# Kernel tuning notes

Hardware: AMD Instinct MI355X
Metric: run time of the kernel (lower is better)

The kernel has to match this reference:

```python
import jax, jax.numpy as jnp
import numpy as np

GAMMA = 0.99
NUM_QUANTILES = 50
STEP_TYPE_LAST = 2
HUBER_DELTA = 1.0

T, B, Q = 128, 512, NUM_QUANTILES


def setup_inputs() -> dict:
    key = jax.random.key(0)
    k1, k2, k3, k4, k5 = jax.random.split(key, 5)
    return {
        "reward": jax.random.normal(k1, (T, B), dtype=jnp.float32),
        "step_type": jax.random.randint(k2, (T, B), 0, 3, dtype=jnp.int32),
        "discount": jax.random.uniform(k3, (T, B), dtype=jnp.float32),
        "value": jax.random.normal(k4, (T, B, Q), dtype=jnp.float32),
        "target_value": jax.random.normal(k5, (T, B, Q), dtype=jnp.float32),
    }


def discounted_return(rewards, values, step_types, discounts):
    """alf value_ops.discounted_return: backward-in-time recurrence.

    rewards/step_types/discounts: [T, B]; values: [T, B, Q].
    Returns [T-1, B, Q]. rets[T-1]=values[T-1];
    rets[t] = is_last[t]*values[t] + (1-is_last[t])*(discounts[t+1]*rets[t+1] + rewards[t+1]).
    """
    is_last = (step_types == STEP_TYPE_LAST).astype(values.dtype)[..., None]  # [T,B,1]
    r = rewards[..., None]    # [T,B,1]
    d = discounts[..., None]  # [T,B,1]

    def step(carry, xs):
        is_last_t, v_t, r_tp1, d_tp1 = xs
        acc = carry * d_tp1 + r_tp1
        ret = is_last_t * v_t + (1.0 - is_last_t) * acc
        return ret, ret

    init = values[-1]
    xs = (is_last[:-1], values[:-1], r[1:], d[1:])
    _, rets = jax.lax.scan(step, init, xs, reverse=True)
    return rets  # [T-1, B, Q]


def huber(x):
    ax = jnp.abs(x)
    return jnp.where(ax <= HUBER_DELTA, 0.5 * x * x, HUBER_DELTA * (ax - 0.5 * HUBER_DELTA))


def reference(reward, step_type, discount, value, target_value):
    # td_lambda == 1.0 -> full discounted return (computed with no grad / detached)
    returns = jax.lax.stop_gradient(
        discounted_return(reward, target_value, step_type, discount * GAMMA))  # [T-1,B,Q]
    v = value[:-1]  # [T-1,B,Q]

    q = returns.shape[-1]
    tau = (jnp.arange(q, dtype=value.dtype) + 0.5) / q  # [Q] cdf midpoints

    # diff[..., i, j] = target_quantile_i - estimated_quantile_j
    diff = returns[..., :, None] - v[..., None, :]  # [T-1,B,Qt,Qe]
    weight = jnp.abs(tau - (jax.lax.stop_gradient(diff) < 0).astype(diff.dtype))
    loss = weight * huber(diff)
    # sum_over_quantiles=True: mean over target quantiles, sum over estimate quantiles
    loss = loss.mean(axis=-2).sum(axis=-1)  # [T-1,B]
    # tensor_extend_zero: append a zero row for the last time step -> [T,B]
    loss = jnp.concatenate([loss, jnp.zeros_like(loss[-1:])], axis=0)
    return loss
```

## Files before the change

### kernel.cpp

```cpp
#include <hip/hip_runtime.h>

#define GAMMA 0.99f
constexpr int T_DIM = 128;
constexpr int B_DIM = 512;
constexpr int Q_DIM = 50;
constexpr int NROW  = (T_DIM - 1) * B_DIM;
constexpr int SLOT  = 52;
constexpr int R_BLK = 20;
constexpr int KEEP  = -1;
constexpr int GRID_LOSS = (NROW + R_BLK - 1) / R_BLK;

__global__ void __launch_bounds__(128) coeff_kernel(
    const float* __restrict__ reward,
    const int*   __restrict__ step_type,
    const float* __restrict__ discount,
    float* __restrict__ alpha,
    float* __restrict__ beta,
    int*   __restrict__ anchor,
    float* __restrict__ out) {
  __shared__ float sp[128], sqa[128], sqb[128];
  __shared__ int   snv[128];
  const int t = threadIdx.x;
  const int b = blockIdx.x;

  float p, qa, qb; int nv;
  if (t < T_DIM - 1) {
    const bool  last = (step_type[t * B_DIM + b] == 2);
    const float d    = GAMMA * discount[(t + 1) * B_DIM + b];
    const float r    = reward[(t + 1) * B_DIM + b];
    p  = last ? 0.0f : d;
    qa = last ? 1.0f : 0.0f;
    qb = last ? 0.0f : r;
    nv = last ? t    : KEEP;
  } else {
    p = 1.0f; qa = 0.0f; qb = 0.0f; nv = KEEP;
    out[(T_DIM - 1) * B_DIM + b] = 0.0f;
  }
  sp[t] = p; sqa[t] = qa; sqb[t] = qb; snv[t] = nv;
  __syncthreads();

#pragma unroll
  for (int off = 1; off < 128; off <<= 1) {
    const bool act = (t + off) < 128;
    float p2 = 1.0f, qa2 = 0.0f, qb2 = 0.0f; int nv2 = KEEP;
    if (act) { p2 = sp[t+off]; qa2 = sqa[t+off]; qb2 = sqb[t+off]; nv2 = snv[t+off]; }
    __syncthreads();
    if (act) {
      qa = fmaf(p, qa2, qa);
      qb = fmaf(p, qb2, qb);
      p  = p * p2;
      nv = (nv == KEEP) ? nv2 : nv;
      sp[t] = p; sqa[t] = qa; sqb[t] = qb; snv[t] = nv;
    }
    __syncthreads();
  }

  if (t < T_DIM - 1) {
    const int row = (b << 7) + t;
    alpha[row]  = p + qa;
    beta[row]   = qb;
    anchor[row] = (nv == KEEP) ? (T_DIM - 1) : nv;
  }
}

__global__ void __launch_bounds__(256) loss_kernel(
    const float* __restrict__ value,
    const float* __restrict__ tv,
    const float* __restrict__ alpha,
    const float* __restrict__ beta,
    const int*   __restrict__ anchor,
    float*       __restrict__ out) {
  __shared__ __align__(16) float sret[R_BLK * SLOT];
  __shared__ float pacc[R_BLK * SLOT];

  const int tid = threadIdx.x;
  const int r0  = blockIdx.x * R_BLK;

  for (int e = tid; e < R_BLK * Q_DIM; e += 256) {
    const int lr  = e / Q_DIM;
    const int i   = e - lr * Q_DIM;
    const int row = r0 + lr;
    float rv = 0.0f;
    if (row < NROW) {
      const int b  = row & (B_DIM - 1);
      const int t  = row >> 9;
      const int ci = (b << 7) + t;
      const int n  = anchor[ci];
      rv = fmaf(alpha[ci], tv[(n * B_DIM + b) * Q_DIM + i], beta[ci]);
    }
    sret[lr * SLOT + i] = rv;
  }
  __syncthreads();

  const bool act   = tid < 5 * Q_DIM;
  const int  r_off = tid / Q_DIM;
  const int  j     = tid - r_off * Q_DIM;
  const float tm05 = ((float)j + 0.5f) * (1.0f / Q_DIM) - 0.5f;

  if (act) {
    float vv[4];
#pragma unroll
    for (int rb = 0; rb < 4; ++rb)
      vv[rb] = value[(r0 + rb * 5) * Q_DIM + tid];

#pragma unroll
    for (int rb = 0; rb < 4; ++rb) {
      const int lr = rb * 5 + r_off;
      const float* rp = &sret[lr * SLOT];
      const float v = vv[rb];

      float s1 = 0.0f, s2 = 0.0f;
      auto pair = [&](float reti) {
        const float d = reti - v;
        const float c = __builtin_amdgcn_fmed3f(d, -1.0f, 1.0f);
        const float e = fmaf(-0.5f, c, d);
        s1 = fmaf(e, c, s1);
        s2 = fmaf(e, fabsf(c), s2);
      };
#pragma unroll
      for (int i0 = 0; i0 < 48; i0 += 4) {
        const float4 rr = *reinterpret_cast<const float4*>(rp + i0);
        pair(rr.x); pair(rr.y); pair(rr.z); pair(rr.w);
      }
      {
        const float2 rr = *reinterpret_cast<const float2*>(rp + 48);
        pair(rr.x); pair(rr.y);
      }
      pacc[lr * SLOT + j] = fmaf(tm05, s2, 0.5f * s1);
    }
  }
  __syncthreads();

  const int w    = tid >> 6;
  const int lane = tid & 63;
#pragma unroll
  for (int k = 0; k < 5; ++k) {
    const int lr   = w * 5 + k;
    const int grow = r0 + lr;
    float x = (lane < Q_DIM) ? pacc[lr * SLOT + lane] : 0.0f;
#pragma unroll
    for (int off = 32; off > 0; off >>= 1)
      x += __shfl_xor(x, off, 64);
    if (lane == 0 && grow < NROW)
      out[grow] = x * (1.0f / Q_DIM);
  }
}

extern "C" void kernel_launch(void* const* d_in, const int* in_sizes, int n_in,
                              void* d_out, int out_size, void* d_ws, size_t ws_size,
                              hipStream_t stream) {
  const float* reward       = (const float*)d_in[0];
  const int*   step_type    = (const int*)  d_in[1];
  const float* discount     = (const float*)d_in[2];
  const float* value        = (const float*)d_in[3];
  const float* target_value = (const float*)d_in[4];
  float* out = (float*)d_out;

  float* alpha  = (float*)d_ws;
  float* beta   = alpha + B_DIM * 128;
  int*   anchor = (int*)(beta + B_DIM * 128);

  coeff_kernel<<<B_DIM, 128, 0, stream>>>(reward, step_type, discount,
                                          alpha, beta, anchor, out);

  loss_kernel<<<GRID_LOSS, 256, 0, stream>>>(value, target_value,
                                             alpha, beta, anchor, out);
}
```

Before: 101.5 us.

## Fuse coefficient scan and quantile loss into one per-batch kernel

Merges the coefficient prefix-scan kernel and the loss kernel into a single kernel with one 1024-thread block per batch column. Alpha, beta and anchor now stay in shared memory, so the workspace round trip and the second launch go away. Each block computes all 127 time steps for its batch index. In exchange the grid shrinks to 512 large blocks using about 53KB of LDS, which limits occupancy. The value and target_value accesses also become strided across time within a block.

```diff
diff --git a/kernel.cpp b/kernel.cpp
--- a/kernel.cpp
+++ b/kernel.cpp
@@ -4,145 +4,115 @@
 constexpr int T_DIM = 128;
 constexpr int B_DIM = 512;
 constexpr int Q_DIM = 50;
-constexpr int NROW  = (T_DIM - 1) * B_DIM;
+constexpr int TRET  = 127;
 constexpr int SLOT  = 52;
-constexpr int R_BLK = 20;
+constexpr int NSLOT = TRET * Q_DIM;
 constexpr int KEEP  = -1;
-constexpr int GRID_LOSS = (NROW + R_BLK - 1) / R_BLK;
 
-__global__ void __launch_bounds__(128) coeff_kernel(
+__global__ void __launch_bounds__(1024) fused_kernel(
     const float* __restrict__ reward,
     const int*   __restrict__ step_type,
     const float* __restrict__ discount,
-    float* __restrict__ alpha,
-    float* __restrict__ beta,
-    int*   __restrict__ anchor,
-    float* __restrict__ out) {
+    const float* __restrict__ value,
+    const float* __restrict__ tv,
+    float*       __restrict__ out) {
+  __shared__ __align__(16) float sret[TRET * SLOT];
+  __shared__ float pacc[TRET * SLOT];
   __shared__ float sp[128], sqa[128], sqb[128];
   __shared__ int   snv[128];
-  const int t = threadIdx.x;
-  const int b = blockIdx.x;
+  __shared__ float s_alpha[TRET], s_beta[TRET];
+  __shared__ int   s_anchor[TRET];
 
-  float p, qa, qb; int nv;
-  if (t < T_DIM - 1) {
-    const bool  last = (step_type[t * B_DIM + b] == 2);
-    const float d    = GAMMA * discount[(t + 1) * B_DIM + b];
-    const float r    = reward[(t + 1) * B_DIM + b];
+  const int tid = threadIdx.x;
+  const int b   = blockIdx.x;
+
+  float p = 1.0f, qa = 0.0f, qb = 0.0f; int nv = KEEP;
+  if (tid < TRET) {
+    const bool  last = (step_type[tid * B_DIM + b] == 2);
+    const float d    = GAMMA * discount[(tid + 1) * B_DIM + b];
+    const float r    = reward[(tid + 1) * B_DIM + b];
     p  = last ? 0.0f : d;
     qa = last ? 1.0f : 0.0f;
     qb = last ? 0.0f : r;
-    nv = last ? t    : KEEP;
-  } else {
-    p = 1.0f; qa = 0.0f; qb = 0.0f; nv = KEEP;
-    out[(T_DIM - 1) * B_DIM + b] = 0.0f;
+    nv = last ? tid  : KEEP;
+  } else if (tid == TRET) {
+    out[TRET * B_DIM + b] = 0.0f;
   }
-  sp[t] = p; sqa[t] = qa; sqb[t] = qb; snv[t] = nv;
+  if (tid < 128) { sp[tid] = p; sqa[tid] = qa; sqb[tid] = qb; snv[tid] = nv; }
   __syncthreads();
 
 #pragma unroll
   for (int off = 1; off < 128; off <<= 1) {
-    const bool act = (t + off) < 128;
+    const bool act = (tid < 128) && (tid + off < 128);
     float p2 = 1.0f, qa2 = 0.0f, qb2 = 0.0f; int nv2 = KEEP;
-    if (act) { p2 = sp[t+off]; qa2 = sqa[t+off]; qb2 = sqb[t+off]; nv2 = snv[t+off]; }
+    if (act) { p2 = sp[tid+off]; qa2 = sqa[tid+off]; qb2 = sqb[tid+off]; nv2 = snv[tid+off]; }
     __syncthreads();
     if (act) {
       qa = fmaf(p, qa2, qa);
       qb = fmaf(p, qb2, qb);
       p  = p * p2;
       nv = (nv == KEEP) ? nv2 : nv;
-      sp[t] = p; sqa[t] = qa; sqb[t] = qb; snv[t] = nv;
+      sp[tid] = p; sqa[tid] = qa; sqb[tid] = qb; snv[tid] = nv;
     }
     __syncthreads();
   }
 
-  if (t < T_DIM - 1) {
-    const int row = (b << 7) + t;
-    alpha[row]  = p + qa;
-    beta[row]   = qb;
-    anchor[row] = (nv == KEEP) ? (T_DIM - 1) : nv;
-  }
-}
-
-__global__ void __launch_bounds__(256) loss_kernel(
-    const float* __restrict__ value,
-    const float* __restrict__ tv,
-    const float* __restrict__ alpha,
-    const float* __restrict__ beta,
-    const int*   __restrict__ anchor,
-    float*       __restrict__ out) {
-  __shared__ __align__(16) float sret[R_BLK * SLOT];
-  __shared__ float pacc[R_BLK * SLOT];
-
-  const int tid = threadIdx.x;
-  const int r0  = blockIdx.x * R_BLK;
-
-  for (int e = tid; e < R_BLK * Q_DIM; e += 256) {
-    const int lr  = e / Q_DIM;
-    const int i   = e - lr * Q_DIM;
-    const int row = r0 + lr;
-    float rv = 0.0f;
-    if (row < NROW) {
-      const int b  = row & (B_DIM - 1);
-      const int t  = row >> 9;
-      const int ci = (b << 7) + t;
-      const int n  = anchor[ci];
-      rv = fmaf(alpha[ci], tv[(n * B_DIM + b) * Q_DIM + i], beta[ci]);
-    }
-    sret[lr * SLOT + i] = rv;
+  if (tid < TRET) {
+    s_alpha[tid]  = p + qa;
+    s_beta[tid]   = qb;
+    s_anchor[tid] = (nv == KEEP) ? TRET : nv;
   }
   __syncthreads();
 
-  const bool act   = tid < 5 * Q_DIM;
-  const int  r_off = tid / Q_DIM;
-  const int  j     = tid - r_off * Q_DIM;
-  const float tm05 = ((float)j + 0.5f) * (1.0f / Q_DIM) - 0.5f;
+  for (int e = tid; e < NSLOT; e += 1024) {
+    const int t = e / Q_DIM;
+    const int i = e - t * Q_DIM;
+    const int n = s_anchor[t];
+    sret[t * SLOT + i] =
+        fmaf(s_alpha[t], tv[(n * B_DIM + b) * Q_DIM + i], s_beta[t]);
+  }
+  __syncthreads();
 
-  if (act) {
-    float vv[4];
+  for (int s = tid; s < NSLOT; s += 1024) {
+    const int t = s / Q_DIM;
+    const int j = s - t * Q_DIM;
+    const float v    = value[(t * B_DIM + b) * Q_DIM + j];
+    const float tm05 = ((float)j + 0.5f) * (1.0f / Q_DIM) - 0.5f;
+    const float* rp  = &sret[t * SLOT];
+
+    float s1 = 0.0f, s2 = 0.0f;
+    auto pair = [&](float reti) {
+      const float d = reti - v;
+      const float c = __builtin_amdgcn_fmed3f(d, -1.0f, 1.0f);
+      const float e = fmaf(-0.5f, c, d);
+      s1 = fmaf(e, c, s1);
+      s2 = fmaf(e, fabsf(c), s2);
+    };
 #pragma unroll
-    for (int rb = 0; rb < 4; ++rb)
-      vv[rb] = value[(r0 + rb * 5) * Q_DIM + tid];
-
-#pragma unroll
-    for (int rb = 0; rb < 4; ++rb) {
-      const int lr = rb * 5 + r_off;
-      const float* rp = &sret[lr * SLOT];
-      const float v = vv[rb];
-
-      float s1 = 0.0f, s2 = 0.0f;
-      auto pair = [&](float reti) {
-        const float d = reti - v;
-        const float c = __builtin_amdgcn_fmed3f(d, -1.0f, 1.0f);
-        const float e = fmaf(-0.5f, c, d);
-        s1 = fmaf(e, c, s1);
-        s2 = fmaf(e, fabsf(c), s2);
-      };
-#pragma unroll
-      for (int i0 = 0; i0 < 48; i0 += 4) {
-        const float4 rr = *reinterpret_cast<const float4*>(rp + i0);
-        pair(rr.x); pair(rr.y); pair(rr.z); pair(rr.w);
-      }
-      {
-        const float2 rr = *reinterpret_cast<const float2*>(rp + 48);
-        pair(rr.x); pair(rr.y);
-      }
-      pacc[lr * SLOT + j] = fmaf(tm05, s2, 0.5f * s1);
+    for (int i0 = 0; i0 < 48; i0 += 4) {
+      const float4 rr = *reinterpret_cast<const float4*>(rp + i0);
+      pair(rr.x); pair(rr.y); pair(rr.z); pair(rr.w);
     }
+    {
+      const float2 rr = *reinterpret_cast<const float2*>(rp + 48);
+      pair(rr.x); pair(rr.y);
+    }
+    pacc[t * SLOT + j] = fmaf(tm05, s2, 0.5f * s1);
   }
   __syncthreads();
 
   const int w    = tid >> 6;
   const int lane = tid & 63;
 #pragma unroll
-  for (int k = 0; k < 5; ++k) {
-    const int lr   = w * 5 + k;
-    const int grow = r0 + lr;
-    float x = (lane < Q_DIM) ? pacc[lr * SLOT + lane] : 0.0f;
+  for (int k = 0; k < 8; ++k) {
+    const int t = w * 8 + k;
+    if (t < TRET) {
+      float x = (lane < Q_DIM) ? pacc[t * SLOT + lane] : 0.0f;
 #pragma unroll
-    for (int off = 32; off > 0; off >>= 1)
-      x += __shfl_xor(x, off, 64);
-    if (lane == 0 && grow < NROW)
-      out[grow] = x * (1.0f / Q_DIM);
+      for (int off = 32; off > 0; off >>= 1)
+        x += __shfl_xor(x, off, 64);
+      if (lane == 0) out[t * B_DIM + b] = x * (1.0f / Q_DIM);
+    }
   }
 }
 
@@ -156,13 +126,6 @@
   const float* target_value = (const float*)d_in[4];
   float* out = (float*)d_out;
 
-  float* alpha  = (float*)d_ws;
-  float* beta   = alpha + B_DIM * 128;
-  int*   anchor = (int*)(beta + B_DIM * 128);
-
-  coeff_kernel<<<B_DIM, 128, 0, stream>>>(reward, step_type, discount,
-                                          alpha, beta, anchor, out);
-
-  loss_kernel<<<GRID_LOSS, 256, 0, stream>>>(value, target_value,
-                                             alpha, beta, anchor, out);
+  fused_kernel<<<B_DIM, 1024, 0, stream>>>(reward, step_type, discount,
+                                           value, target_value, out);
 }
```

Result: no change. 101.4 us (-0.0%).
